# Kernel optimization log

Measured on AMD Instinct MI355X. Metric: run time of the kernel, lower is better.

The kernel has to match this reference:

```python
import jax, jax.numpy as jnp
import numpy as np

N_NODES = 100000
N_EDGES = 1600000
D_IN = 128
D_HID = 64


def setup_inputs() -> dict:
    key = jax.random.key(0)
    k1, k2, k3, k4 = jax.random.split(key, 4)
    x = jax.random.normal(k1, (N_NODES, D_IN), dtype=jnp.float32)
    edge_index = jax.random.randint(k2, (2, N_EDGES), 0, N_NODES, dtype=jnp.int64)
    W1 = jax.random.normal(k3, (D_IN, D_HID), dtype=jnp.float32) / np.sqrt(D_IN)
    b1 = jnp.zeros((D_HID,), dtype=jnp.float32)
    W2 = jax.random.normal(k4, (D_HID, 1), dtype=jnp.float32) / np.sqrt(D_HID)
    b2 = jnp.zeros((1,), dtype=jnp.float32)
    return {"x": x, "edge_index": edge_index, "W1": W1, "b1": b1, "W2": W2, "b2": b2}


def _gcn_layer(x, W, b, src, dst, norm, n):
    # PyG GCNConv: linear transform, then normalized scatter-add aggregation, then bias
    h = x @ W                                   # [N, d_out]
    msg = h[src] * norm[:, None]                # gather + edge-weight   [E', d_out]
    out = jax.ops.segment_sum(msg, dst, num_segments=n)  # scatter-add
    return out + b


def reference(x, edge_index, W1, b1, W2, b2):
    n = x.shape[0]
    loops = jnp.arange(n, dtype=edge_index.dtype)
    src = jnp.concatenate([edge_index[0], loops])  # self-loops added (GCN default)
    dst = jnp.concatenate([edge_index[1], loops])
    # symmetric normalization: deg^{-1/2}[src] * deg^{-1/2}[dst]
    deg = jax.ops.segment_sum(jnp.ones(dst.shape, x.dtype), dst, num_segments=n)
    dis = jnp.where(deg > 0, jax.lax.rsqrt(jnp.maximum(deg, 1e-12)), 0.0)
    norm = dis[src] * dis[dst]
    h = jax.nn.relu(_gcn_layer(x, W1, b1, src, dst, norm, n))
    y = _gcn_layer(h, W2, b2, src, dst, norm, n)   # [N, 1]
    # ConstantPad1d((0, num_node_features-1), 0) -> [N, D_IN]
    return jnp.pad(y, ((0, 0), (0, x.shape[1] - 1)))
```

## Files before the change

kernel.cpp:

```cpp
#include <hip/hip_runtime.h>

#define N_NODES 100000
#define N_EDGES 1600000
#define D_IN 128
#define D_HID 64

#define BKT_SHIFT 8
#define BKT_NODES 256
#define NB 391
#define NBLK 392
#define SLOT 32
#define SEG4 (SLOT / 4)
#define REG4 (NBLK * SEG4)
#define SLOTS_PB (NBLK * SLOT)
#define BKT_CAP 5120
#define OVF_CAP 8192

#define EST 1024
#define BST 1024

typedef __attribute__((ext_vector_type(8))) short bf16x8;
typedef __attribute__((ext_vector_type(4))) float f32x4;

__device__ __forceinline__ unsigned short f2b(float f) {
    union { float f; unsigned u; } c; c.f = f;
    unsigned r = (c.u + 0x7FFFu + ((c.u >> 16) & 1u)) >> 16;
    return (unsigned short)r;
}
__device__ __forceinline__ float blo(unsigned u) { return __uint_as_float(u << 16); }
__device__ __forceinline__ float bhi(unsigned u) { return __uint_as_float(u & 0xffff0000u); }

__global__ __launch_bounds__(256) void k_prep(const float* __restrict__ W1,
                                              unsigned short* __restrict__ w1t,
                                              int* __restrict__ ovf_cnt) {
    int t = blockIdx.x * 256 + threadIdx.x;
    if (t == 0) ovf_cnt[0] = 0;
    int k = t >> 6, f = t & 63;
    w1t[f * D_IN + k] = f2b(W1[t]);
}

__global__ __launch_bounds__(EST) void k_escatter(const int* __restrict__ src,
                                                  const int* __restrict__ dst,
                                                  int* __restrict__ pairs,
                                                  int* __restrict__ cnt_blk,
                                                  int* __restrict__ ovf_cnt,
                                                  int2* __restrict__ ovf, int E) {
    __shared__ int lcur[NB];
    int tid = threadIdx.x;
    for (int t = tid; t < NB; t += EST) lcur[t] = 0;
    __syncthreads();
    int chunk = (E + NBLK - 1) / NBLK;
    int beg = blockIdx.x * chunk;
    int end = min(beg + chunk, E);
    for (int e = beg + tid; e < end; e += EST) {
        int d = dst[e], s = src[e];
        int bk = d >> BKT_SHIFT;
        int slot = atomicAdd(&lcur[bk], 1);
        if (slot < SLOT)
            pairs[(bk * NBLK + blockIdx.x) * SLOT + slot] = (s << BKT_SHIFT) | (d & (BKT_NODES - 1));
        else {
            int o = atomicAdd(ovf_cnt, 1);
            if (o < OVF_CAP) ovf[o] = make_int2(s, d);
        }
    }
    __syncthreads();
    for (int t = tid; t < NB; t += EST)
        cnt_blk[t * NBLK + blockIdx.x] = min(lcur[t], SLOT);
}

__global__ __launch_bounds__(BST) void k_bsort(const uint4* __restrict__ pairs4,
                                               const int* __restrict__ cnt_blk,
                                               const int* __restrict__ ovf_cnt,
                                               const int2* __restrict__ ovf,
                                               int* __restrict__ srcs_sorted,
                                               int* __restrict__ row_start,
                                               int* __restrict__ row_end,
                                               float* __restrict__ dis, int n) {
    __shared__ uint4 reg4[REG4];
    __shared__ int segc[NBLK];
    __shared__ int cnt[BKT_NODES];
    __shared__ int exc[BKT_NODES];
    __shared__ int sorted[BKT_CAP];
    __shared__ int nE_sh;
    int b = blockIdx.x;
    int tid = threadIdx.x;
    int node0 = b << BKT_SHIFT;
    int ocnt = min(ovf_cnt[0], OVF_CAP);
    const uint4* region = pairs4 + (size_t)b * REG4;

    for (int i = tid; i < REG4; i += BST) reg4[i] = region[i];
    for (int i = tid; i < NBLK; i += BST) segc[i] = cnt_blk[b * NBLK + i];
    if (tid < BKT_NODES) cnt[tid] = 0;
    __syncthreads();

    for (int i4 = tid; i4 < REG4; i4 += BST) {
        uint4 v = reg4[i4];
        int c = segc[i4 >> 3];
        int k = (i4 & 7) * 4;
        if (k < c)     atomicAdd(&cnt[v.x & (BKT_NODES - 1)], 1);
        if (k + 1 < c) atomicAdd(&cnt[v.y & (BKT_NODES - 1)], 1);
        if (k + 2 < c) atomicAdd(&cnt[v.z & (BKT_NODES - 1)], 1);
        if (k + 3 < c) atomicAdd(&cnt[v.w & (BKT_NODES - 1)], 1);
    }
    for (int k = tid; k < ocnt; k += BST) {
        int2 e = ovf[k];
        if ((e.y >> BKT_SHIFT) == b) atomicAdd(&cnt[e.y & (BKT_NODES - 1)], 1);
    }
    __syncthreads();

    if (tid < 64) {
        int run = 0;
        for (int c = 0; c < BKT_NODES; c += 64) {
            int v = cnt[c + tid];
            int inc = v;
            for (int off = 1; off < 64; off <<= 1) {
                int t2 = __shfl_up(inc, off);
                if (tid >= off) inc += t2;
            }
            exc[c + tid] = run + inc - v;
            run += __shfl(inc, 63);
        }
        if (tid == 63) nE_sh = run;
    }
    __syncthreads();

    if (tid < BKT_NODES) {
        int node = node0 + tid;
        if (node < n) {
            int rs = b * BKT_CAP + exc[tid];
            row_start[node] = rs;
            row_end[node] = rs + cnt[tid];
            dis[node] = rsqrtf((float)cnt[tid] + 1.0f);
        }
    }
    int nE = nE_sh;
    __syncthreads();
    if (tid < BKT_NODES) cnt[tid] = exc[tid];
    __syncthreads();

    for (int i4 = tid; i4 < REG4; i4 += BST) {
        uint4 v = reg4[i4];
        int c = segc[i4 >> 3];
        int k = (i4 & 7) * 4;
        if (k < c)     { int p = atomicAdd(&cnt[v.x & (BKT_NODES - 1)], 1); sorted[p] = v.x >> BKT_SHIFT; }
        if (k + 1 < c) { int p = atomicAdd(&cnt[v.y & (BKT_NODES - 1)], 1); sorted[p] = v.y >> BKT_SHIFT; }
        if (k + 2 < c) { int p = atomicAdd(&cnt[v.z & (BKT_NODES - 1)], 1); sorted[p] = v.z >> BKT_SHIFT; }
        if (k + 3 < c) { int p = atomicAdd(&cnt[v.w & (BKT_NODES - 1)], 1); sorted[p] = v.w >> BKT_SHIFT; }
    }
    for (int k = tid; k < ocnt; k += BST) {
        int2 e = ovf[k];
        if ((e.y >> BKT_SHIFT) == b) {
            int p = atomicAdd(&cnt[e.y & (BKT_NODES - 1)], 1);
            sorted[p] = e.x;
        }
    }
    __syncthreads();

    int gbase = b * BKT_CAP;
    for (int k = tid; k < nE; k += BST)
        srcs_sorted[gbase + k] = sorted[k];
}

#define LS 136
__global__ __launch_bounds__(256) void k_gemm1(const float* __restrict__ x,
                                               const uint4* __restrict__ w1t4,
                                               const float* __restrict__ dis,
                                               unsigned short* __restrict__ h1s, int n) {
    __shared__ unsigned short xs[64 * LS];
    __shared__ unsigned short ws[64 * LS];
    int tid = threadIdx.x;
    int node0 = blockIdx.x * 64;

#pragma unroll
    for (int it = 0; it < 4; ++it) {
        int e = tid + it * 256;
        int f = e >> 4, c = e & 15;
        *(uint4*)&ws[f * LS + c * 8] = w1t4[e];
    }
#pragma unroll
    for (int it = 0; it < 8; ++it) {
        int e4 = tid + it * 256;
        int node = e4 >> 5;
        int k = (e4 & 31) * 4;
        float4 v = make_float4(0.f, 0.f, 0.f, 0.f);
        if (node0 + node < n)
            v = ((const float4*)x)[((size_t)(node0 + node) * D_IN + k) >> 2];
        uint2 u;
        u.x = (unsigned)f2b(v.x) | ((unsigned)f2b(v.y) << 16);
        u.y = (unsigned)f2b(v.z) | ((unsigned)f2b(v.w) << 16);
        *(uint2*)&xs[node * LS + k] = u;
    }
    __syncthreads();

    int wv = tid >> 6;
    int lane = tid & 63;
    int m16 = lane & 15;
    int q = lane >> 4;

    bf16x8 afrag[4];
#pragma unroll
    for (int ks = 0; ks < 4; ++ks)
        afrag[ks] = *(const bf16x8*)&xs[(wv * 16 + m16) * LS + ks * 32 + q * 8];

    f32x4 acc[4];
#pragma unroll
    for (int ft = 0; ft < 4; ++ft) acc[ft] = (f32x4){0.f, 0.f, 0.f, 0.f};

#pragma unroll
    for (int ft = 0; ft < 4; ++ft)
#pragma unroll
        for (int ks = 0; ks < 4; ++ks) {
            bf16x8 bfrag = *(const bf16x8*)&ws[(ft * 16 + m16) * LS + ks * 32 + q * 8];
            acc[ft] = __builtin_amdgcn_mfma_f32_16x16x32_bf16(afrag[ks], bfrag, acc[ft], 0, 0, 0);
        }

#pragma unroll
    for (int r = 0; r < 4; ++r) {
        int node = node0 + wv * 16 + q * 4 + r;
        if (node < n) {
            float d = dis[node];
#pragma unroll
            for (int ft = 0; ft < 4; ++ft)
                h1s[(size_t)node * D_HID + ft * 16 + m16] = f2b(acc[ft][r] * d);
        }
    }
}

__global__ __launch_bounds__(256) void k_gather1(const int* __restrict__ srcs,
                                                 const int* __restrict__ row_start,
                                                 const int* __restrict__ row_end,
                                                 const float* __restrict__ dis,
                                                 const uint4* __restrict__ h4,
                                                 const float* __restrict__ b1,
                                                 const float* __restrict__ W2,
                                                 float* __restrict__ zd, int n) {
    int i = blockIdx.x * 8 + (threadIdx.x >> 5);
    int lane = threadIdx.x & 63;
    int g = (lane >> 3) & 3;
    int m8 = lane & 7;
    float dd = dis[i];

    float a0, a1, a2, a3, a4, a5, a6, a7;
    {
        uint4 u = h4[(unsigned)i * 8u + m8];
        float w = (g == 0) ? 1.f : 0.f;
        a0 = w * blo(u.x); a1 = w * bhi(u.x);
        a2 = w * blo(u.y); a3 = w * bhi(u.y);
        a4 = w * blo(u.z); a5 = w * bhi(u.z);
        a6 = w * blo(u.w); a7 = w * bhi(u.w);
    }

#define ACC(u) { a0 += blo(u.x); a1 += bhi(u.x); a2 += blo(u.y); a3 += bhi(u.y); \
                 a4 += blo(u.z); a5 += bhi(u.z); a6 += blo(u.w); a7 += bhi(u.w); }
    int end = row_end[i];
    int j = row_start[i] + g;
    for (; j + 4 < end; j += 8) {
        int s0 = srcs[j];
        int s1 = srcs[j + 4];
        uint4 u0 = h4[(unsigned)s0 * 8u + m8];
        uint4 u1 = h4[(unsigned)s1 * 8u + m8];
        ACC(u0); ACC(u1);
    }
    if (j < end) {
        int s0 = srcs[j];
        uint4 u0 = h4[(unsigned)s0 * 8u + m8];
        ACC(u0);
    }
#undef ACC

#pragma unroll
    for (int off = 8; off < 32; off <<= 1) {
        a0 += __shfl_xor(a0, off); a1 += __shfl_xor(a1, off);
        a2 += __shfl_xor(a2, off); a3 += __shfl_xor(a3, off);
        a4 += __shfl_xor(a4, off); a5 += __shfl_xor(a5, off);
        a6 += __shfl_xor(a6, off); a7 += __shfl_xor(a7, off);
    }
    float4 ba = ((const float4*)b1)[m8 * 2];
    float4 bb = ((const float4*)b1)[m8 * 2 + 1];
    float4 wa = ((const float4*)W2)[m8 * 2];
    float4 wb = ((const float4*)W2)[m8 * 2 + 1];
    float v = fmaxf(fmaf(dd, a0, ba.x), 0.f) * wa.x + fmaxf(fmaf(dd, a1, ba.y), 0.f) * wa.y
            + fmaxf(fmaf(dd, a2, ba.z), 0.f) * wa.z + fmaxf(fmaf(dd, a3, ba.w), 0.f) * wa.w
            + fmaxf(fmaf(dd, a4, bb.x), 0.f) * wb.x + fmaxf(fmaf(dd, a5, bb.y), 0.f) * wb.y
            + fmaxf(fmaf(dd, a6, bb.z), 0.f) * wb.z + fmaxf(fmaf(dd, a7, bb.w), 0.f) * wb.w;
#pragma unroll
    for (int off = 1; off < 8; off <<= 1) v += __shfl_xor(v, off);
    if ((lane & 31) == 0) zd[i] = v * dd;
}

__global__ __launch_bounds__(256) void k_gather2(const int* __restrict__ srcs,
                                                 const int* __restrict__ row_start,
                                                 const int* __restrict__ row_end,
                                                 const float* __restrict__ dis,
                                                 const float* __restrict__ zd,
                                                 const float* __restrict__ b2,
                                                 float* __restrict__ out, int n) {
    int i = blockIdx.x * 8 + (threadIdx.x >> 5);
    int l = threadIdx.x & 31;
    float acc = 0.f;
    int beg = row_start[i], end = row_end[i];
    for (int j = beg + l; j < end; j += 32)
        acc += zd[srcs[j]];
#pragma unroll
    for (int off = 1; off < 32; off <<= 1) acc += __shfl_xor(acc, off);
    float y = (acc + zd[i]) * dis[i] + b2[0];
    float4 v = make_float4(0.f, 0.f, 0.f, 0.f);
    if (l == 0) v.x = y;
    ((float4*)out)[(size_t)i * 32 + l] = v;
}

extern "C" void kernel_launch(void* const* d_in, const int* in_sizes, int n_in,
                              void* d_out, int out_size, void* d_ws, size_t ws_size,
                              hipStream_t stream) {
    const float* x  = (const float*)d_in[0];
    const int*   ei = (const int*)d_in[1];
    const float* W1 = (const float*)d_in[2];
    const float* b1 = (const float*)d_in[3];
    const float* W2 = (const float*)d_in[4];
    const float* b2 = (const float*)d_in[5];
    float* out = (float*)d_out;

    const int n = N_NODES;
    const int E = N_EDGES;
    const int* src = ei;
    const int* dst = ei + E;

    int* pairs       = (int*)d_ws;
    int* cnt_blk     = pairs + (size_t)NB * NBLK * SLOT;
    int* srcs_sorted = cnt_blk + (size_t)NB * NBLK;
    int* row_start   = srcs_sorted + (size_t)NB * BKT_CAP;
    int* row_end     = row_start + n;
    int* ovf_cnt     = row_end + n;
    int2* ovf        = (int2*)(ovf_cnt + 4);
    float* dis       = (float*)(ovf + OVF_CAP);
    unsigned short* h1s = (unsigned short*)(dis + n);
    unsigned short* w1t = h1s + (size_t)n * D_HID;
    float* zd        = (float*)(w1t + D_IN * D_HID);

    k_prep<<<32, 256, 0, stream>>>(W1, w1t, ovf_cnt);
    k_escatter<<<NBLK, EST, 0, stream>>>(src, dst, pairs, cnt_blk, ovf_cnt, ovf, E);
    k_bsort<<<NB, BST, 0, stream>>>((const uint4*)pairs, cnt_blk, ovf_cnt, ovf,
                                    srcs_sorted, row_start, row_end, dis, n);

    k_gemm1<<<(n + 63) / 64, 256, 0, stream>>>(x, (const uint4*)w1t, dis, h1s, n);

    k_gather1<<<(n + 7) / 8, 256, 0, stream>>>(srcs_sorted, row_start, row_end, dis,
                                               (const uint4*)h1s, b1, W2, zd, n);
    k_gather2<<<(n + 7) / 8, 256, 0, stream>>>(srcs_sorted, row_start, row_end, dis,
                                               zd, b2, out, n);
}
```

Measured before the change: 206.1 us.

## Split hidden features into two halves gathered in separate passes

The GEMM now writes the 64-wide bf16 hidden table as two 32-wide halves, and the first-layer gather runs as two kernels, each aggregating one half and accumulating its partial layer-2 projection. The intent is to shrink the randomly gathered working set per pass so it fits better in cache. In exchange, the edge index lists and row offsets are read twice and an extra kernel launch is added.

```diff
diff --git a/kernel.cpp b/kernel.cpp
--- a/kernel.cpp
+++ b/kernel.cpp
@@ -12,7 +12,6 @@
 #define SLOT 32
 #define SEG4 (SLOT / 4)
 #define REG4 (NBLK * SEG4)
-#define SLOTS_PB (NBLK * SLOT)
 #define BKT_CAP 5120
 #define OVF_CAP 8192
 
@@ -165,7 +164,8 @@
 __global__ __launch_bounds__(256) void k_gemm1(const float* __restrict__ x,
                                                const uint4* __restrict__ w1t4,
                                                const float* __restrict__ dis,
-                                               unsigned short* __restrict__ h1s, int n) {
+                                               unsigned short* __restrict__ h1L,
+                                               unsigned short* __restrict__ h1H, int n) {
     __shared__ unsigned short xs[64 * LS];
     __shared__ unsigned short ws[64 * LS];
     int tid = threadIdx.x;
@@ -220,72 +220,93 @@
         if (node < n) {
             float d = dis[node];
 #pragma unroll
-            for (int ft = 0; ft < 4; ++ft)
-                h1s[(size_t)node * D_HID + ft * 16 + m16] = f2b(acc[ft][r] * d);
-        }
-    }
-}
-
-__global__ __launch_bounds__(256) void k_gather1(const int* __restrict__ srcs,
-                                                 const int* __restrict__ row_start,
-                                                 const int* __restrict__ row_end,
-                                                 const float* __restrict__ dis,
-                                                 const uint4* __restrict__ h4,
-                                                 const float* __restrict__ b1,
-                                                 const float* __restrict__ W2,
-                                                 float* __restrict__ zd, int n) {
+            for (int ft = 0; ft < 4; ++ft) {
+                unsigned short* dst = (ft < 2) ? h1L : h1H;
+                dst[(size_t)node * 32 + (ft & 1) * 16 + m16] = f2b(acc[ft][r] * d);
+            }
+        }
+    }
+}
+
+__device__ __forceinline__ void gather_half(const int* __restrict__ srcs,
+                                            const int* __restrict__ row_start,
+                                            const int* __restrict__ row_end,
+                                            const float* __restrict__ dis,
+                                            const uint2* __restrict__ h2,
+                                            const float* __restrict__ b1h,
+                                            const float* __restrict__ W2h,
+                                            const float* __restrict__ zprev,
+                                            float* __restrict__ zout) {
     int i = blockIdx.x * 8 + (threadIdx.x >> 5);
     int lane = threadIdx.x & 63;
     int g = (lane >> 3) & 3;
     int m8 = lane & 7;
     float dd = dis[i];
 
-    float a0, a1, a2, a3, a4, a5, a6, a7;
+    float a0, a1, a2, a3;
     {
-        uint4 u = h4[(unsigned)i * 8u + m8];
+        uint2 u = h2[(unsigned)i * 8u + m8];
         float w = (g == 0) ? 1.f : 0.f;
         a0 = w * blo(u.x); a1 = w * bhi(u.x);
         a2 = w * blo(u.y); a3 = w * bhi(u.y);
-        a4 = w * blo(u.z); a5 = w * bhi(u.z);
-        a6 = w * blo(u.w); a7 = w * bhi(u.w);
-    }
-
-#define ACC(u) { a0 += blo(u.x); a1 += bhi(u.x); a2 += blo(u.y); a3 += bhi(u.y); \
-                 a4 += blo(u.z); a5 += bhi(u.z); a6 += blo(u.w); a7 += bhi(u.w); }
+    }
+
+#define ACC4(u) { a0 += blo(u.x); a1 += bhi(u.x); a2 += blo(u.y); a3 += bhi(u.y); }
     int end = row_end[i];
     int j = row_start[i] + g;
     for (; j + 4 < end; j += 8) {
         int s0 = srcs[j];
         int s1 = srcs[j + 4];
-        uint4 u0 = h4[(unsigned)s0 * 8u + m8];
-        uint4 u1 = h4[(unsigned)s1 * 8u + m8];
-        ACC(u0); ACC(u1);
+        uint2 u0 = h2[(unsigned)s0 * 8u + m8];
+        uint2 u1 = h2[(unsigned)s1 * 8u + m8];
+        ACC4(u0); ACC4(u1);
     }
     if (j < end) {
         int s0 = srcs[j];
-        uint4 u0 = h4[(unsigned)s0 * 8u + m8];
-        ACC(u0);
-    }
-#undef ACC
+        uint2 u0 = h2[(unsigned)s0 * 8u + m8];
+        ACC4(u0);
+    }
+#undef ACC4
 
 #pragma unroll
     for (int off = 8; off < 32; off <<= 1) {
         a0 += __shfl_xor(a0, off); a1 += __shfl_xor(a1, off);
         a2 += __shfl_xor(a2, off); a3 += __shfl_xor(a3, off);
-        a4 += __shfl_xor(a4, off); a5 += __shfl_xor(a5, off);
-        a6 += __shfl_xor(a6, off); a7 += __shfl_xor(a7, off);
-    }
-    float4 ba = ((const float4*)b1)[m8 * 2];
-    float4 bb = ((const float4*)b1)[m8 * 2 + 1];
-    float4 wa = ((const float4*)W2)[m8 * 2];
-    float4 wb = ((const float4*)W2)[m8 * 2 + 1];
+    }
+    float4 ba = ((const float4*)b1h)[m8];
+    float4 wa = ((const float4*)W2h)[m8];
     float v = fmaxf(fmaf(dd, a0, ba.x), 0.f) * wa.x + fmaxf(fmaf(dd, a1, ba.y), 0.f) * wa.y
-            + fmaxf(fmaf(dd, a2, ba.z), 0.f) * wa.z + fmaxf(fmaf(dd, a3, ba.w), 0.f) * wa.w
-            + fmaxf(fmaf(dd, a4, bb.x), 0.f) * wb.x + fmaxf(fmaf(dd, a5, bb.y), 0.f) * wb.y
-            + fmaxf(fmaf(dd, a6, bb.z), 0.f) * wb.z + fmaxf(fmaf(dd, a7, bb.w), 0.f) * wb.w;
+            + fmaxf(fmaf(dd, a2, ba.z), 0.f) * wa.z + fmaxf(fmaf(dd, a3, ba.w), 0.f) * wa.w;
 #pragma unroll
     for (int off = 1; off < 8; off <<= 1) v += __shfl_xor(v, off);
-    if ((lane & 31) == 0) zd[i] = v * dd;
+    if ((lane & 31) == 0) {
+        float z = v * dd;
+        if (zprev) z += zprev[i];
+        zout[i] = z;
+    }
+}
+
+__global__ __launch_bounds__(256) void k_gather1L(const int* __restrict__ srcs,
+                                                  const int* __restrict__ row_start,
+                                                  const int* __restrict__ row_end,
+                                                  const float* __restrict__ dis,
+                                                  const uint2* __restrict__ h2L,
+                                                  const float* __restrict__ b1,
+                                                  const float* __restrict__ W2,
+                                                  float* __restrict__ zdl) {
+    gather_half(srcs, row_start, row_end, dis, h2L, b1, W2, nullptr, zdl);
+}
+
+__global__ __launch_bounds__(256) void k_gather1H(const int* __restrict__ srcs,
+                                                  const int* __restrict__ row_start,
+                                                  const int* __restrict__ row_end,
+                                                  const float* __restrict__ dis,
+                                                  const uint2* __restrict__ h2H,
+                                                  const float* __restrict__ b1,
+                                                  const float* __restrict__ W2,
+                                                  const float* __restrict__ zdl,
+                                                  float* __restrict__ zd) {
+    gather_half(srcs, row_start, row_end, dis, h2H, b1 + 32, W2 + 32, zdl, zd);
 }
 
 __global__ __launch_bounds__(256) void k_gather2(const int* __restrict__ srcs,
@@ -333,19 +354,23 @@
     int* ovf_cnt     = row_end + n;
     int2* ovf        = (int2*)(ovf_cnt + 4);
     float* dis       = (float*)(ovf + OVF_CAP);
-    unsigned short* h1s = (unsigned short*)(dis + n);
-    unsigned short* w1t = h1s + (size_t)n * D_HID;
-    float* zd        = (float*)(w1t + D_IN * D_HID);
+    unsigned short* h1L = (unsigned short*)(dis + n);
+    unsigned short* h1H = h1L + (size_t)n * 32;
+    unsigned short* w1t = h1H + (size_t)n * 32;
+    float* zdl       = (float*)(w1t + D_IN * D_HID);
+    float* zd        = zdl + n;
 
     k_prep<<<32, 256, 0, stream>>>(W1, w1t, ovf_cnt);
     k_escatter<<<NBLK, EST, 0, stream>>>(src, dst, pairs, cnt_blk, ovf_cnt, ovf, E);
     k_bsort<<<NB, BST, 0, stream>>>((const uint4*)pairs, cnt_blk, ovf_cnt, ovf,
                                     srcs_sorted, row_start, row_end, dis, n);
 
-    k_gemm1<<<(n + 63) / 64, 256, 0, stream>>>(x, (const uint4*)w1t, dis, h1s, n);
-
-    k_gather1<<<(n + 7) / 8, 256, 0, stream>>>(srcs_sorted, row_start, row_end, dis,
-                                               (const uint4*)h1s, b1, W2, zd, n);
+    k_gemm1<<<(n + 63) / 64, 256, 0, stream>>>(x, (const uint4*)w1t, dis, h1L, h1H, n);
+
+    k_gather1L<<<(n + 7) / 8, 256, 0, stream>>>(srcs_sorted, row_start, row_end, dis,
+                                                (const uint2*)h1L, b1, W2, zdl);
+    k_gather1H<<<(n + 7) / 8, 256, 0, stream>>>(srcs_sorted, row_start, row_end, dis,
+                                                (const uint2*)h1H, b1, W2, zdl, zd);
     k_gather2<<<(n + 7) / 8, 256, 0, stream>>>(srcs_sorted, row_start, row_end, dis,
                                                zd, b2, out, n);
 }
```

Result: slower. 223.1 us (+8.3%).

## Stage edge-scatter in LDS, skip empty slots, phase aggregation gathers by source range

Applied to the files above, without the earlier changes.

The edge scatter kernel now buffers bucketed pairs in shared memory and writes only filled 16-byte segments to global memory with coalesced stores. The sort kernel loads only the valid segments of its region. The layer-1 aggregation loop is split into four passes, each gathering only sources within a 25000-node range, so the working set of h held in cache at any moment is smaller. This costs re-reading the edge index lists four times and adds divergent branches in the gather loop.

```diff
diff --git a/kernel.cpp b/kernel.cpp
--- a/kernel.cpp
+++ b/kernel.cpp
@@ -12,12 +12,14 @@
 #define SLOT 32
 #define SEG4 (SLOT / 4)
 #define REG4 (NBLK * SEG4)
-#define SLOTS_PB (NBLK * SLOT)
 #define BKT_CAP 5120
 #define OVF_CAP 8192
 
-#define EST 1024
+#define EST 512
 #define BST 1024
+
+#define NPH 4
+#define PHSZ 25000u
 
 typedef __attribute__((ext_vector_type(8))) short bf16x8;
 typedef __attribute__((ext_vector_type(4))) float f32x4;
@@ -46,6 +48,7 @@
                                                   int* __restrict__ ovf_cnt,
                                                   int2* __restrict__ ovf, int E) {
     __shared__ int lcur[NB];
+    __shared__ int lp[NB * SLOT];
     int tid = threadIdx.x;
     for (int t = tid; t < NB; t += EST) lcur[t] = 0;
     __syncthreads();
@@ -57,13 +60,21 @@
         int bk = d >> BKT_SHIFT;
         int slot = atomicAdd(&lcur[bk], 1);
         if (slot < SLOT)
-            pairs[(bk * NBLK + blockIdx.x) * SLOT + slot] = (s << BKT_SHIFT) | (d & (BKT_NODES - 1));
+            lp[(bk << 5) + slot] = (s << BKT_SHIFT) | (d & (BKT_NODES - 1));
         else {
             int o = atomicAdd(ovf_cnt, 1);
             if (o < OVF_CAP) ovf[o] = make_int2(s, d);
         }
     }
     __syncthreads();
+    uint4* p4 = (uint4*)pairs;
+    const uint4* lp4 = (const uint4*)lp;
+    for (int i4 = tid; i4 < NB * SEG4; i4 += EST) {
+        int bk = i4 >> 3;
+        int c = min(lcur[bk], SLOT);
+        if (((i4 & 7) << 2) < c)
+            p4[((size_t)bk * NBLK + blockIdx.x) * SEG4 + (i4 & 7)] = lp4[i4];
+    }
     for (int t = tid; t < NB; t += EST)
         cnt_blk[t * NBLK + blockIdx.x] = min(lcur[t], SLOT);
 }
@@ -88,19 +99,21 @@
     int ocnt = min(ovf_cnt[0], OVF_CAP);
     const uint4* region = pairs4 + (size_t)b * REG4;
 
-    for (int i = tid; i < REG4; i += BST) reg4[i] = region[i];
     for (int i = tid; i < NBLK; i += BST) segc[i] = cnt_blk[b * NBLK + i];
     if (tid < BKT_NODES) cnt[tid] = 0;
     __syncthreads();
 
     for (int i4 = tid; i4 < REG4; i4 += BST) {
-        uint4 v = reg4[i4];
         int c = segc[i4 >> 3];
         int k = (i4 & 7) * 4;
-        if (k < c)     atomicAdd(&cnt[v.x & (BKT_NODES - 1)], 1);
-        if (k + 1 < c) atomicAdd(&cnt[v.y & (BKT_NODES - 1)], 1);
-        if (k + 2 < c) atomicAdd(&cnt[v.z & (BKT_NODES - 1)], 1);
-        if (k + 3 < c) atomicAdd(&cnt[v.w & (BKT_NODES - 1)], 1);
+        if (k < c) {
+            uint4 v = region[i4];
+            reg4[i4] = v;
+            atomicAdd(&cnt[v.x & (BKT_NODES - 1)], 1);
+            if (k + 1 < c) atomicAdd(&cnt[v.y & (BKT_NODES - 1)], 1);
+            if (k + 2 < c) atomicAdd(&cnt[v.z & (BKT_NODES - 1)], 1);
+            if (k + 3 < c) atomicAdd(&cnt[v.w & (BKT_NODES - 1)], 1);
+        }
     }
     for (int k = tid; k < ocnt; k += BST) {
         int2 e = ovf[k];
@@ -139,13 +152,15 @@
     __syncthreads();
 
     for (int i4 = tid; i4 < REG4; i4 += BST) {
-        uint4 v = reg4[i4];
         int c = segc[i4 >> 3];
         int k = (i4 & 7) * 4;
-        if (k < c)     { int p = atomicAdd(&cnt[v.x & (BKT_NODES - 1)], 1); sorted[p] = v.x >> BKT_SHIFT; }
-        if (k + 1 < c) { int p = atomicAdd(&cnt[v.y & (BKT_NODES - 1)], 1); sorted[p] = v.y >> BKT_SHIFT; }
-        if (k + 2 < c) { int p = atomicAdd(&cnt[v.z & (BKT_NODES - 1)], 1); sorted[p] = v.z >> BKT_SHIFT; }
-        if (k + 3 < c) { int p = atomicAdd(&cnt[v.w & (BKT_NODES - 1)], 1); sorted[p] = v.w >> BKT_SHIFT; }
+        if (k < c) {
+            uint4 v = reg4[i4];
+            { int p = atomicAdd(&cnt[v.x & (BKT_NODES - 1)], 1); sorted[p] = v.x >> BKT_SHIFT; }
+            if (k + 1 < c) { int p = atomicAdd(&cnt[v.y & (BKT_NODES - 1)], 1); sorted[p] = v.y >> BKT_SHIFT; }
+            if (k + 2 < c) { int p = atomicAdd(&cnt[v.z & (BKT_NODES - 1)], 1); sorted[p] = v.z >> BKT_SHIFT; }
+            if (k + 3 < c) { int p = atomicAdd(&cnt[v.w & (BKT_NODES - 1)], 1); sorted[p] = v.w >> BKT_SHIFT; }
+        }
     }
     for (int k = tid; k < ocnt; k += BST) {
         int2 e = ovf[k];
@@ -252,19 +267,23 @@
 
 #define ACC(u) { a0 += blo(u.x); a1 += bhi(u.x); a2 += blo(u.y); a3 += bhi(u.y); \
                  a4 += blo(u.z); a5 += bhi(u.z); a6 += blo(u.w); a7 += bhi(u.w); }
+    int beg = row_start[i];
     int end = row_end[i];
-    int j = row_start[i] + g;
-    for (; j + 4 < end; j += 8) {
-        int s0 = srcs[j];
-        int s1 = srcs[j + 4];
-        uint4 u0 = h4[(unsigned)s0 * 8u + m8];
-        uint4 u1 = h4[(unsigned)s1 * 8u + m8];
-        ACC(u0); ACC(u1);
-    }
-    if (j < end) {
-        int s0 = srcs[j];
-        uint4 u0 = h4[(unsigned)s0 * 8u + m8];
-        ACC(u0);
+    for (int ph = 0; ph < NPH; ++ph) {
+        unsigned lo = ph * PHSZ;
+        int j = beg + g;
+        for (; j + 4 < end; j += 8) {
+            unsigned s0 = (unsigned)srcs[j];
+            unsigned s1 = (unsigned)srcs[j + 4];
+            bool t0 = (s0 - lo) < PHSZ;
+            bool t1 = (s1 - lo) < PHSZ;
+            if (t0) { uint4 u0 = h4[s0 * 8u + m8]; ACC(u0); }
+            if (t1) { uint4 u1 = h4[s1 * 8u + m8]; ACC(u1); }
+        }
+        if (j < end) {
+            unsigned s0 = (unsigned)srcs[j];
+            if ((s0 - lo) < PHSZ) { uint4 u0 = h4[s0 * 8u + m8]; ACC(u0); }
+        }
     }
 #undef ACC
 
```

Result: slower. 240.1 us (+16.5%).
